# Kernel tuning notes

Measured on AMD Instinct MI355X. Metric: run time of the kernel, lower is better.

Reference implementation:

```python
import jax, jax.numpy as jnp
import numpy as np

B, T, C, H, WIN = 1, 2048, 512, 8, 48
DH = C // H  # 64


def setup_inputs() -> dict:
    key = jax.random.key(0)
    kx, kq, ko, kp = jax.random.split(key, 4)
    x = jax.random.normal(kx, (B, T, C), dtype=jnp.float32)
    W_qkv = jax.random.normal(kq, (C, 3 * C), dtype=jnp.float32) / np.sqrt(C).astype(np.float32)
    W_out = jax.random.normal(ko, (C, C), dtype=jnp.float32) / np.sqrt(C).astype(np.float32)
    # one random cycle permutation per head: perms[h, pi_pos] = original_pos
    perms = jax.vmap(lambda k: jax.random.permutation(k, T))(jax.random.split(kp, H)).astype(jnp.int32)
    return {"x": x, "W_qkv": W_qkv, "W_out": W_out, "perms": perms}


def _head_attn(qh, kh, vh, perm):
    # qh, kh, vh: [B, T, DH]; perm: [T] with perm[pi_pos] = original_pos
    Tn = perm.shape[0]
    inv_perm = jnp.argsort(perm)  # inv_perm[orig_pos] = pi_pos
    q_pi = qh[:, perm]
    k_pi = kh[:, perm]
    v_pi = vh[:, perm]
    offs = jnp.arange(-WIN, WIN + 1)                      # [W]
    pi_idx = jnp.arange(Tn)[:, None] + offs[None, :]      # [T, W]
    idx = jnp.clip(pi_idx, 0, Tn - 1)
    k_win = k_pi[:, idx]                                  # [B, T, W, DH]
    v_win = v_pi[:, idx]                                  # [B, T, W, DH]
    scores = jnp.einsum('btd,btwd->btw', q_pi, k_win) / np.sqrt(DH).astype(np.float32)
    neigh_orig = perm[idx]                                # [T, W] original positions of neighbors
    mask = (neigh_orig <= perm[:, None]) & (pi_idx >= 0) & (pi_idx < Tn)  # causal + window validity
    scores = jnp.where(mask[None], scores, jnp.finfo(scores.dtype).min)
    w = jax.nn.softmax(scores, axis=-1)                   # [B, T, W]
    y_pi = jnp.einsum('btw,btwd->btd', w, v_win)          # [B, T, DH]
    return y_pi[:, inv_perm]                              # back to original order


def reference(x, W_qkv, W_out, perms):
    qkv = x @ W_qkv                                       # [B, T, 3C]
    q, k, v = jnp.split(qkv, 3, axis=-1)
    q = q.reshape(B, T, H, DH)
    k = k.reshape(B, T, H, DH)
    v = v.reshape(B, T, H, DH)
    # heads are independent; vmap over head axis with per-head permutation
    y = jax.vmap(_head_attn, in_axes=(2, 2, 2, 0), out_axes=2)(q, k, v, perms)  # [B, T, H, DH]
    return y.reshape(B, T, C) @ W_out
```

## Files before the change

### kernel.cpp

```cpp
#include <hip/hip_runtime.h>
#include <float.h>
#include <math.h>

#define T_DIM 2048
#define C_DIM 512
#define QKV_LD 1536
#define NBLK 512

typedef float f32x4 __attribute__((ext_vector_type(4)));
typedef short s16x8 __attribute__((ext_vector_type(8)));

__device__ __forceinline__ unsigned short f2bf(float f) {
  unsigned u = __float_as_uint(f);
  return (unsigned short)((u + 0x7fffu + ((u >> 16) & 1u)) >> 16);
}
__device__ __forceinline__ float bflo(unsigned u) { return __uint_as_float(u << 16); }

__device__ __forceinline__ void load16_to_lds(const void* g, void* l) {
  __builtin_amdgcn_global_load_lds(
      (const __attribute__((address_space(1))) unsigned int*)g,
      (__attribute__((address_space(3))) unsigned int*)(unsigned int)(unsigned long long)l,
      16, 0, 0);
}

__global__ __launch_bounds__(256) void prep_kernel(const float* __restrict__ x,
                                                   const float* __restrict__ Wqkv,
                                                   const float* __restrict__ Wout,
                                                   unsigned short* __restrict__ xbf,
                                                   unsigned short* __restrict__ WqkvT,
                                                   unsigned short* __restrict__ WoutT) {
  __shared__ float tile[32][33];
  const int tid = threadIdx.x, bid = blockIdx.x;

  const float4* xs4 = (const float4*)x;
  for (int i = bid * 256 + tid; i < (T_DIM * C_DIM) / 4; i += NBLK * 256) {
    float4 v = xs4[i];
    ushort4 o;
    o.x = f2bf(v.x); o.y = f2bf(v.y); o.z = f2bf(v.z); o.w = f2bf(v.w);
    ((ushort4*)xbf)[i] = o;
  }
  const int tx = tid & 31, ty = tid >> 5;
  for (int tt = bid; tt < 1024; tt += NBLK) {
    const float* src; unsigned short* dst; int Cc, R, bx, by;
    if (tt < 768) { src = Wqkv; dst = WqkvT; Cc = QKV_LD; R = C_DIM; bx = (tt % 48) * 32; by = (tt / 48) * 32; }
    else { int u = tt - 768; src = Wout; dst = WoutT; Cc = C_DIM; R = C_DIM; bx = (u & 15) * 32; by = (u >> 4) * 32; }
    __syncthreads();
#pragma unroll
    for (int i = 0; i < 4; ++i) { int r = ty + i * 8; tile[r][tx] = src[(size_t)(by + r) * Cc + bx + tx]; }
    __syncthreads();
#pragma unroll
    for (int i = 0; i < 4; ++i) { int r = ty + i * 8; dst[(size_t)(bx + r) * R + by + tx] = f2bf(tile[tx][r]); }
  }
}

template <int BM, int BN, bool OUT16>
__device__ __forceinline__ void gemm_body(const unsigned short* __restrict__ A,
                                          const unsigned short* __restrict__ BT,
                                          void* __restrict__ Cp,
                                          int N, int K, int tilesX,
                                          unsigned short* lA, unsigned short* lB,
                                          int tid, int bid) {
  constexpr int BK = 32;
  constexpr int BM2 = BM / 2, BN2 = BN / 2;
  constexpr int MT = BM2 / 16, NT = BN2 / 16;
  constexpr int IA = BM / 64;
  constexpr int IB = BN / 64;
  const int lane = tid & 63, w = tid >> 6, wr = w >> 1, wc = w & 1;
  const int fm = lane & 15, q8 = (lane >> 4) * 8, q4 = lane >> 4;

  const int m0 = (bid / tilesX) * BM, n0 = (bid % tilesX) * BN;
  f32x4 acc[MT][NT] = {};
  for (int k0 = 0; k0 < K; k0 += BK) {
    __syncthreads();
#pragma unroll
    for (int i = 0; i < IA; ++i) {
      int chunk = i * 256 + tid, row = chunk >> 2, c8 = (chunk & 3) * 8;
      load16_to_lds(&A[(size_t)(m0 + row) * K + k0 + c8], lA + chunk * 8);
    }
#pragma unroll
    for (int i = 0; i < IB; ++i) {
      int chunk = i * 256 + tid, row = chunk >> 2, c8 = (chunk & 3) * 8;
      load16_to_lds(&BT[(size_t)(n0 + row) * K + k0 + c8], lB + chunk * 8);
    }
    __syncthreads();
    s16x8 a[MT], b[NT];
#pragma unroll
    for (int mi = 0; mi < MT; ++mi)
      a[mi] = *(const s16x8*)&lA[(wr * BM2 + mi * 16 + fm) * BK + q8];
#pragma unroll
    for (int ni = 0; ni < NT; ++ni)
      b[ni] = *(const s16x8*)&lB[(wc * BN2 + ni * 16 + fm) * BK + q8];
#pragma unroll
    for (int mi = 0; mi < MT; ++mi)
#pragma unroll
      for (int ni = 0; ni < NT; ++ni)
        acc[mi][ni] = __builtin_amdgcn_mfma_f32_16x16x32_bf16(a[mi], b[ni], acc[mi][ni], 0, 0, 0);
  }
#pragma unroll
  for (int mi = 0; mi < MT; ++mi)
#pragma unroll
    for (int ni = 0; ni < NT; ++ni)
#pragma unroll
      for (int r = 0; r < 4; ++r) {
        int row = m0 + wr * BM2 + mi * 16 + q4 * 4 + r;
        int col = n0 + wc * BN2 + ni * 16 + fm;
        if constexpr (OUT16)
          ((unsigned short*)Cp)[(size_t)row * N + col] = f2bf(acc[mi][ni][r]);
        else
          ((float*)Cp)[(size_t)row * N + col] = acc[mi][ni][r];
      }
}

__global__ __launch_bounds__(256) void gemm1_kernel(const unsigned short* __restrict__ A,
                                                    const unsigned short* __restrict__ BT,
                                                    unsigned short* __restrict__ Cc) {
  __shared__ __align__(16) unsigned short smem[(128 + 64) * 32];
  gemm_body<128, 64, true>(A, BT, Cc, QKV_LD, C_DIM, 24, smem, smem + 128 * 32,
                           threadIdx.x, blockIdx.x);
}
__global__ __launch_bounds__(256) void gemm2_kernel(const unsigned short* __restrict__ A,
                                                    const unsigned short* __restrict__ BT,
                                                    float* __restrict__ Cc) {
  __shared__ __align__(16) unsigned short smem[(64 + 64) * 32];
  gemm_body<64, 64, false>(A, BT, Cc, C_DIM, C_DIM, 8, smem, smem + 64 * 32,
                           threadIdx.x, blockIdx.x);
}

__global__ __launch_bounds__(256) void attn_kernel(const unsigned short* __restrict__ qkvbf,
                                                   const int* __restrict__ perms,
                                                   unsigned short* __restrict__ Ybf) {
  __shared__ __align__(16) unsigned char smem[48768];
  int* ow            = (int*)smem;
  unsigned short* lQ = (unsigned short*)(smem + 512);
  unsigned short* lK = (unsigned short*)(smem + 5120);
  float* Sb          = (float*)(smem + 23552);
  unsigned short* lP = (unsigned short*)(smem + 40064);
  unsigned short* lVT= (unsigned short*)(smem + 5120);

  const int tid = threadIdx.x, bid = blockIdx.x;
  const int lane = tid & 63, w = tid >> 6;
  const int fm = lane & 15, q8 = (lane >> 4) * 8, q4 = lane >> 4;
  const int h = bid >> 6;
  const int t0 = (bid & 63) << 5;

  if (tid < 128) {
    int pi = t0 - 48 + tid;
    int idx = min(max(pi, 0), T_DIM - 1);
    ow[tid] = perms[h * T_DIM + idx];
  }
  __syncthreads();

#pragma unroll
  for (int it = 0; it < 4; ++it) {
    int c = it * 256 + tid;
    int row = c >> 3, k8 = c & 7;
    uint4 d = *(const uint4*)(qkvbf + (size_t)ow[row] * QKV_LD + C_DIM + h * 64 + k8 * 8);
    *(uint4*)(lK + row * 72 + k8 * 8) = d;
  }
  {
    int row = tid >> 3, k8 = tid & 7;
    uint4 d = *(const uint4*)(qkvbf + (size_t)ow[48 + row] * QKV_LD + h * 64 + k8 * 8);
    *(uint4*)(lQ + row * 72 + k8 * 8) = d;
  }
  __syncthreads();

  {
    f32x4 accs[2][2] = {};
#pragma unroll
    for (int kt = 0; kt < 2; ++kt) {
      s16x8 aq[2];
#pragma unroll
      for (int mi = 0; mi < 2; ++mi)
        aq[mi] = *(const s16x8*)&lQ[(mi * 16 + fm) * 72 + kt * 32 + q8];
#pragma unroll
      for (int ni = 0; ni < 2; ++ni) {
        s16x8 bk = *(const s16x8*)&lK[(w * 32 + ni * 16 + fm) * 72 + kt * 32 + q8];
#pragma unroll
        for (int mi = 0; mi < 2; ++mi)
          accs[mi][ni] = __builtin_amdgcn_mfma_f32_16x16x32_bf16(aq[mi], bk, accs[mi][ni], 0, 0, 0);
      }
    }
#pragma unroll
    for (int mi = 0; mi < 2; ++mi)
#pragma unroll
      for (int ni = 0; ni < 2; ++ni)
#pragma unroll
        for (int r = 0; r < 4; ++r)
          Sb[(mi * 16 + q4 * 4 + r) * 129 + w * 32 + ni * 16 + fm] = accs[mi][ni][r] * 0.125f;
  }
  __syncthreads();

#pragma unroll
  for (int it = 0; it < 4; ++it) {
    int c = it * 256 + tid;
    int j = c >> 3, d0 = (c & 7) * 8;
    uint4 v = *(const uint4*)(qkvbf + (size_t)ow[j] * QKV_LD + 2 * C_DIM + h * 64 + d0);
    lVT[(d0 + 0) * 136 + j] = (unsigned short)(v.x & 0xffff);
    lVT[(d0 + 1) * 136 + j] = (unsigned short)(v.x >> 16);
    lVT[(d0 + 2) * 136 + j] = (unsigned short)(v.y & 0xffff);
    lVT[(d0 + 3) * 136 + j] = (unsigned short)(v.y >> 16);
    lVT[(d0 + 4) * 136 + j] = (unsigned short)(v.z & 0xffff);
    lVT[(d0 + 5) * 136 + j] = (unsigned short)(v.z >> 16);
    lVT[(d0 + 6) * 136 + j] = (unsigned short)(v.w & 0xffff);
    lVT[(d0 + 7) * 136 + j] = (unsigned short)(v.w >> 16);
  }

  for (int si = 0; si < 8; ++si) {
    const int s = w * 8 + si;
    const int p = ow[48 + s];
    const int c1 = lane + 64;
    const float v0 = Sb[s * 129 + lane];
    const float v1 = Sb[s * 129 + c1];
    const int pi0 = t0 - 48 + lane;
    const bool valid0 = (lane >= s) && (pi0 >= 0) && (pi0 < T_DIM) && (ow[lane] <= p);
    const bool valid1 = (lane <= s + 32) && (pi0 + 64 < T_DIM) && (ow[c1] <= p);
    float mx = fmaxf(valid0 ? v0 : -FLT_MAX, valid1 ? v1 : -FLT_MAX);
#pragma unroll
    for (int off = 32; off > 0; off >>= 1) mx = fmaxf(mx, __shfl_xor(mx, off, 64));
    const float e0 = valid0 ? __expf(v0 - mx) : 0.f;
    const float e1 = valid1 ? __expf(v1 - mx) : 0.f;
    float sum = e0 + e1;
#pragma unroll
    for (int off = 32; off > 0; off >>= 1) sum += __shfl_xor(sum, off, 64);
    const float inv = 1.f / sum;
    lP[s * 136 + lane] = valid0 ? f2bf(e0 * inv) : (unsigned short)0;
    lP[s * 136 + c1]   = valid1 ? f2bf(e1 * inv) : (unsigned short)0;
  }
  __syncthreads();

  {
    const int wr = w >> 1, wc = w & 1;
    f32x4 acco[2] = {};
#pragma unroll
    for (int kt = 0; kt < 4; ++kt) {
      s16x8 ap = *(const s16x8*)&lP[(wr * 16 + fm) * 136 + kt * 32 + q8];
#pragma unroll
      for (int ni = 0; ni < 2; ++ni) {
        s16x8 bv = *(const s16x8*)&lVT[((wc * 2 + ni) * 16 + fm) * 136 + kt * 32 + q8];
        acco[ni] = __builtin_amdgcn_mfma_f32_16x16x32_bf16(ap, bv, acco[ni], 0, 0, 0);
      }
    }
#pragma unroll
    for (int ni = 0; ni < 2; ++ni)
#pragma unroll
      for (int r = 0; r < 4; ++r) {
        int q = wr * 16 + q4 * 4 + r;
        int d = (wc * 2 + ni) * 16 + fm;
        Ybf[(size_t)ow[48 + q] * C_DIM + h * 64 + d] = f2bf(acco[ni][r]);
      }
  }
}

extern "C" void kernel_launch(void* const* d_in, const int* in_sizes, int n_in,
                              void* d_out, int out_size, void* d_ws, size_t ws_size,
                              hipStream_t stream) {
  const float* x     = (const float*)d_in[0];
  const float* Wqkv  = (const float*)d_in[1];
  const float* Wout  = (const float*)d_in[2];
  const int*   perms = (const int*)d_in[3];
  float* out = (float*)d_out;
  unsigned short* ws = (unsigned short*)d_ws;

  unsigned short* xbf   = ws;
  unsigned short* WqkvT = xbf + 1048576;
  unsigned short* WoutT = WqkvT + 786432;
  unsigned short* qkvbf = WoutT + 262144;
  unsigned short* Ybf   = qkvbf + 3145728;

  prep_kernel<<<NBLK, 256, 0, stream>>>(x, Wqkv, Wout, xbf, WqkvT, WoutT);
  gemm1_kernel<<<384, 256, 0, stream>>>(xbf, WqkvT, qkvbf);
  attn_kernel<<<NBLK, 256, 0, stream>>>(qkvbf, perms, Ybf);
  gemm2_kernel<<<256, 256, 0, stream>>>(Ybf, WoutT, out);
}
```

Baseline: 95.65 us.

## Fuse fp32-to-bf16 conversion and weight transpose into GEMM tile loads

Removes the separate prep kernel that converted x and both weight matrices to bf16 and transposed the weights. The GEMMs now read fp32 directly, converting x rows on the fly and loading weight columns per k-slice. The weight tiles are transposed into LDS with an XOR-swizzled layout to avoid bank conflicts. This saves one kernel launch and a full write/read round trip of the converted data. In exchange, each GEMM block re-reads and re-converts fp32 data, and the B loads become strided scalar reads instead of async 16-byte LDS loads.

```diff
diff --git a/kernel.cpp b/kernel.cpp
--- a/kernel.cpp
+++ b/kernel.cpp
@@ -14,7 +14,6 @@
   unsigned u = __float_as_uint(f);
   return (unsigned short)((u + 0x7fffu + ((u >> 16) & 1u)) >> 16);
 }
-__device__ __forceinline__ float bflo(unsigned u) { return __uint_as_float(u << 16); }
 
 __device__ __forceinline__ void load16_to_lds(const void* g, void* l) {
   __builtin_amdgcn_global_load_lds(
@@ -23,64 +22,61 @@
       16, 0, 0);
 }
 
-__global__ __launch_bounds__(256) void prep_kernel(const float* __restrict__ x,
-                                                   const float* __restrict__ Wqkv,
-                                                   const float* __restrict__ Wout,
-                                                   unsigned short* __restrict__ xbf,
-                                                   unsigned short* __restrict__ WqkvT,
-                                                   unsigned short* __restrict__ WoutT) {
-  __shared__ float tile[32][33];
-  const int tid = threadIdx.x, bid = blockIdx.x;
-
-  const float4* xs4 = (const float4*)x;
-  for (int i = bid * 256 + tid; i < (T_DIM * C_DIM) / 4; i += NBLK * 256) {
-    float4 v = xs4[i];
-    ushort4 o;
-    o.x = f2bf(v.x); o.y = f2bf(v.y); o.z = f2bf(v.z); o.w = f2bf(v.w);
-    ((ushort4*)xbf)[i] = o;
-  }
-  const int tx = tid & 31, ty = tid >> 5;
-  for (int tt = bid; tt < 1024; tt += NBLK) {
-    const float* src; unsigned short* dst; int Cc, R, bx, by;
-    if (tt < 768) { src = Wqkv; dst = WqkvT; Cc = QKV_LD; R = C_DIM; bx = (tt % 48) * 32; by = (tt / 48) * 32; }
-    else { int u = tt - 768; src = Wout; dst = WoutT; Cc = C_DIM; R = C_DIM; bx = (u & 15) * 32; by = (u >> 4) * 32; }
-    __syncthreads();
-#pragma unroll
-    for (int i = 0; i < 4; ++i) { int r = ty + i * 8; tile[r][tx] = src[(size_t)(by + r) * Cc + bx + tx]; }
-    __syncthreads();
-#pragma unroll
-    for (int i = 0; i < 4; ++i) { int r = ty + i * 8; dst[(size_t)(bx + r) * R + by + tx] = f2bf(tile[tx][r]); }
-  }
-}
-
-template <int BM, int BN, bool OUT16>
-__device__ __forceinline__ void gemm_body(const unsigned short* __restrict__ A,
-                                          const unsigned short* __restrict__ BT,
+template <int BM, bool AF32, bool OUT16>
+__device__ __forceinline__ void gemm_body(const void* __restrict__ Ap,
+                                          const float* __restrict__ B,
                                           void* __restrict__ Cp,
                                           int N, int K, int tilesX,
                                           unsigned short* lA, unsigned short* lB,
                                           int tid, int bid) {
   constexpr int BK = 32;
-  constexpr int BM2 = BM / 2, BN2 = BN / 2;
-  constexpr int MT = BM2 / 16, NT = BN2 / 16;
-  constexpr int IA = BM / 64;
-  constexpr int IB = BN / 64;
+  constexpr int BM2 = BM / 2, BN2 = 32;
+  constexpr int MT = BM2 / 16, NT = 2;
   const int lane = tid & 63, w = tid >> 6, wr = w >> 1, wc = w & 1;
-  const int fm = lane & 15, q8 = (lane >> 4) * 8, q4 = lane >> 4;
-
-  const int m0 = (bid / tilesX) * BM, n0 = (bid % tilesX) * BN;
+  const int fm = lane & 15, q4 = lane >> 4, q8 = q4 * 8;
+
+  const int m0 = (bid / tilesX) * BM, n0 = (bid % tilesX) * 64;
+  const int bn = lane;
+  const int bslot = w ^ ((bn >> 1) & 3);
+
   f32x4 acc[MT][NT] = {};
   for (int k0 = 0; k0 < K; k0 += BK) {
     __syncthreads();
-#pragma unroll
-    for (int i = 0; i < IA; ++i) {
-      int chunk = i * 256 + tid, row = chunk >> 2, c8 = (chunk & 3) * 8;
-      load16_to_lds(&A[(size_t)(m0 + row) * K + k0 + c8], lA + chunk * 8);
-    }
-#pragma unroll
-    for (int i = 0; i < IB; ++i) {
-      int chunk = i * 256 + tid, row = chunk >> 2, c8 = (chunk & 3) * 8;
-      load16_to_lds(&BT[(size_t)(n0 + row) * K + k0 + c8], lB + chunk * 8);
+    if constexpr (AF32) {
+      const float* A = (const float*)Ap;
+#pragma unroll
+      for (int i = 0; i < BM / 64; ++i) {
+        int c = i * 256 + tid;
+        int row = c >> 2, c8 = (c & 3) * 8;
+        const float* src = &A[(size_t)(m0 + row) * K + k0 + c8];
+        float4 v0 = *(const float4*)src;
+        float4 v1 = *(const float4*)(src + 4);
+        uint4 o;
+        o.x = f2bf(v0.x) | ((unsigned)f2bf(v0.y) << 16);
+        o.y = f2bf(v0.z) | ((unsigned)f2bf(v0.w) << 16);
+        o.z = f2bf(v1.x) | ((unsigned)f2bf(v1.y) << 16);
+        o.w = f2bf(v1.z) | ((unsigned)f2bf(v1.w) << 16);
+        *(uint4*)(lA + row * 32 + c8) = o;
+      }
+    } else {
+      const unsigned short* A = (const unsigned short*)Ap;
+#pragma unroll
+      for (int i = 0; i < BM / 64; ++i) {
+        int c = i * 256 + tid, row = c >> 2, c8 = (c & 3) * 8;
+        load16_to_lds(&A[(size_t)(m0 + row) * K + k0 + c8], lA + c * 8);
+      }
+    }
+    {
+      float f[8];
+#pragma unroll
+      for (int i = 0; i < 8; ++i)
+        f[i] = B[(size_t)(k0 + w * 8 + i) * N + n0 + bn];
+      uint4 o;
+      o.x = f2bf(f[0]) | ((unsigned)f2bf(f[1]) << 16);
+      o.y = f2bf(f[2]) | ((unsigned)f2bf(f[3]) << 16);
+      o.z = f2bf(f[4]) | ((unsigned)f2bf(f[5]) << 16);
+      o.w = f2bf(f[6]) | ((unsigned)f2bf(f[7]) << 16);
+      *(uint4*)(lB + bn * 32 + bslot * 8) = o;
     }
     __syncthreads();
     s16x8 a[MT], b[NT];
@@ -88,8 +84,10 @@
     for (int mi = 0; mi < MT; ++mi)
       a[mi] = *(const s16x8*)&lA[(wr * BM2 + mi * 16 + fm) * BK + q8];
 #pragma unroll
-    for (int ni = 0; ni < NT; ++ni)
-      b[ni] = *(const s16x8*)&lB[(wc * BN2 + ni * 16 + fm) * BK + q8];
+    for (int ni = 0; ni < NT; ++ni) {
+      int row = wc * BN2 + ni * 16 + fm;
+      b[ni] = *(const s16x8*)&lB[row * 32 + ((q4 ^ ((row >> 1) & 3)) * 8)];
+    }
 #pragma unroll
     for (int mi = 0; mi < MT; ++mi)
 #pragma unroll
@@ -111,19 +109,19 @@
       }
 }
 
-__global__ __launch_bounds__(256) void gemm1_kernel(const unsigned short* __restrict__ A,
-                                                    const unsigned short* __restrict__ BT,
-                                                    unsigned short* __restrict__ Cc) {
+__global__ __launch_bounds__(256) void gemm1_kernel(const float* __restrict__ x,
+                                                    const float* __restrict__ Wqkv,
+                                                    unsigned short* __restrict__ qkvbf) {
   __shared__ __align__(16) unsigned short smem[(128 + 64) * 32];
-  gemm_body<128, 64, true>(A, BT, Cc, QKV_LD, C_DIM, 24, smem, smem + 128 * 32,
-                           threadIdx.x, blockIdx.x);
-}
-__global__ __launch_bounds__(256) void gemm2_kernel(const unsigned short* __restrict__ A,
-                                                    const unsigned short* __restrict__ BT,
-                                                    float* __restrict__ Cc) {
+  gemm_body<128, true, true>(x, Wqkv, qkvbf, QKV_LD, C_DIM, 24,
+                             smem, smem + 128 * 32, threadIdx.x, blockIdx.x);
+}
+__global__ __launch_bounds__(256) void gemm2_kernel(const unsigned short* __restrict__ Ybf,
+                                                    const float* __restrict__ Wout,
+                                                    float* __restrict__ out) {
   __shared__ __align__(16) unsigned short smem[(64 + 64) * 32];
-  gemm_body<64, 64, false>(A, BT, Cc, C_DIM, C_DIM, 8, smem, smem + 64 * 32,
-                           threadIdx.x, blockIdx.x);
+  gemm_body<64, false, false>(Ybf, Wout, out, C_DIM, C_DIM, 8,
+                              smem, smem + 64 * 32, threadIdx.x, blockIdx.x);
 }
 
 __global__ __launch_bounds__(256) void attn_kernel(const unsigned short* __restrict__ qkvbf,
@@ -261,14 +259,10 @@
   float* out = (float*)d_out;
   unsigned short* ws = (unsigned short*)d_ws;
 
-  unsigned short* xbf   = ws;
-  unsigned short* WqkvT = xbf + 1048576;
-  unsigned short* WoutT = WqkvT + 786432;
-  unsigned short* qkvbf = WoutT + 262144;
+  unsigned short* qkvbf = ws;
   unsigned short* Ybf   = qkvbf + 3145728;
 
-  prep_kernel<<<NBLK, 256, 0, stream>>>(x, Wqkv, Wout, xbf, WqkvT, WoutT);
-  gemm1_kernel<<<384, 256, 0, stream>>>(xbf, WqkvT, qkvbf);
+  gemm1_kernel<<<384, 256, 0, stream>>>(x, Wqkv, qkvbf);
   attn_kernel<<<NBLK, 256, 0, stream>>>(qkvbf, perms, Ybf);
-  gemm2_kernel<<<256, 256, 0, stream>>>(Ybf, WoutT, out);
-}
+  gemm2_kernel<<<256, 256, 0, stream>>>(Ybf, Wout, out);
+}
```

Result: slower. 104.6 us (+9.3%).
